# Performance work log

Hardware: AMD Instinct MI355X
Metric: run time of the kernel (lower is better)

## Reference

```python
import jax, jax.numpy as jnp
import numpy as np

B, S, D, H = 2, 2048, 1024, 16
DK = D // H


def setup_inputs() -> dict:
    key = jax.random.key(0)
    ks = jax.random.split(key, 12)
    s = 0.02
    return {
        "q": jax.random.normal(ks[0], (B, S, D), jnp.float32),
        "k": jax.random.normal(ks[1], (B, S, D), jnp.float32),
        "v": jax.random.normal(ks[2], (B, S, D), jnp.float32),
        "mask": jax.random.randint(ks[3], (1, 1, S, S), 0, 2, jnp.int32),
        "Wq": jax.random.normal(ks[4], (D, D), jnp.float32) * s,
        "bq": jnp.zeros((D,), jnp.float32),
        "Wk": jax.random.normal(ks[5], (D, D), jnp.float32) * s,
        "bk": jnp.zeros((D,), jnp.float32),
        "Wv": jax.random.normal(ks[6], (D, D), jnp.float32) * s,
        "bv": jnp.zeros((D,), jnp.float32),
        "Wo": jax.random.normal(ks[7], (D, D), jnp.float32) * s,
        "bo": jnp.zeros((D,), jnp.float32),
    }


def reference(q, k, v, mask, Wq, bq, Wk, bk, Wv, bv, Wo, bo):
    # linear projections (torch Linear: x @ W.T + b)
    qp = q @ Wq.T + bq
    kp = k @ Wk.T + bk
    vp = v @ Wv.T + bv
    # [B, S, D] -> [B, H, S, DK]
    split = lambda x: x.reshape(B, S, H, DK).transpose(0, 2, 1, 3)
    qh, kh, vh = split(qp), split(kp), split(vp)
    scale = 1.0 / jnp.sqrt(jnp.float32(DK))
    attn = jnp.einsum('bhsd,bhtd->bhst', qh, kh) * scale  # [B,H,S,S]
    attn = jnp.where(mask == 0, jnp.float32(-1e9), attn)
    attn = jax.nn.softmax(attn, axis=-1)
    out = jnp.einsum('bhst,bhtd->bhsd', attn, vh)  # [B,H,S,DK]
    concat = out.transpose(0, 2, 1, 3).reshape(B, S, D)
    return concat @ Wo.T + bo
```

## Files before the change

kernel.cpp:

```cpp
#include <hip/hip_runtime.h>
#include <hip/hip_bf16.h>


using bf16x8 = __attribute__((ext_vector_type(8))) short;
using f32x4  = __attribute__((ext_vector_type(4))) float;

constexpr int Bc = 2, Sc = 2048, Dc = 1024, Hc = 16, DKc = 64;
constexpr int Mc = Bc * Sc;
#define QSCALE 0.18033688011112042f

__device__ __forceinline__ void lds_load16(const void* g, void* l) {
  __builtin_amdgcn_global_load_lds(
      (const __attribute__((address_space(1))) unsigned int*)g,
      (__attribute__((address_space(3))) unsigned int*)l, 16, 0, 0);
}

#if __has_builtin(__builtin_amdgcn_exp2f)
__device__ __forceinline__ float exp2_fast(float x) { return __builtin_amdgcn_exp2f(x); }
#else
__device__ __forceinline__ float exp2_fast(float x) {
  float r;
  asm("v_exp_f32 %0, %1\n\ts_nop 0" : "=v"(r) : "v"(x));
  return r;
}
#endif

__device__ __forceinline__ unsigned pack_trunc(float a, float b) {
  return __builtin_amdgcn_perm(__float_as_uint(b), __float_as_uint(a), 0x07060302u);
}

__device__ __forceinline__ unsigned pack2bf(float a, float b) {
  union { __hip_bfloat16 h; unsigned short s; } ua, ub;
  ua.h = __float2bfloat16(a);
  ub.h = __float2bfloat16(b);
  return (unsigned)ua.s | ((unsigned)ub.s << 16);
}

__global__ void prep(const float* __restrict__ q, const float* __restrict__ k,
                     const float* __restrict__ v, const int* __restrict__ mask,
                     const float* __restrict__ Wq, const float* __restrict__ Wk,
                     const float* __restrict__ Wv, const float* __restrict__ Wo,
                     char* __restrict__ ws) {
  const size_t MB = 1024 * 1024;
  int blk = blockIdx.x;
  if (blk < 12288) {
    int which = blk >> 12;
    int i = (((blk & 4095) << 8) + threadIdx.x) * 4;
    const float* s = which == 0 ? q : (which == 1 ? k : v);
    __hip_bfloat16* d = (__hip_bfloat16*)(ws + (size_t)which * 8 * MB);
    float4 x = *(const float4*)&s[i];
    uint2 pk = {pack2bf(x.x, x.y), pack2bf(x.z, x.w)};
    *(uint2*)&d[i] = pk;
  } else if (blk < 16384) {
    int bb = blk - 12288;
    int which = bb >> 10;
    int i = (((bb & 1023) << 8) + threadIdx.x) * 4;
    const float* s = which == 0 ? Wq : (which == 1 ? Wk : (which == 2 ? Wv : Wo));
    __hip_bfloat16* d = which < 3 ? (__hip_bfloat16*)(ws + (24 + 2 * which) * MB)
                                  : (__hip_bfloat16*)(ws + 30 * MB);
    float4 x = *(const float4*)&s[i];
    uint2 pk = {pack2bf(x.x, x.y), pack2bf(x.z, x.w)};
    *(uint2*)&d[i] = pk;
  } else {
    int i = ((blk - 16384) << 8) + threadIdx.x;
    unsigned long long bal = __ballot(mask[i] != 0);
    if ((threadIdx.x & 63) == 0)
      ((unsigned long long*)(ws + 32 * MB))[i >> 6] = bal;
  }
}

__global__ __launch_bounds__(256, 3) void proj_qkv(
    const __hip_bfloat16* __restrict__ qb, const __hip_bfloat16* __restrict__ kb,
    const __hip_bfloat16* __restrict__ vb, const __hip_bfloat16* __restrict__ Wcat,
    const float* __restrict__ bq, const float* __restrict__ bk,
    const float* __restrict__ bv, __hip_bfloat16* __restrict__ qhd,
    __hip_bfloat16* __restrict__ khd, __hip_bfloat16* __restrict__ vtd) {
  __shared__ __align__(16) __hip_bfloat16 As[2][128 * 32];
  __shared__ __align__(16) __hip_bfloat16 Bs[2][128 * 32];
  const int tid = threadIdx.x;
  const int f = blockIdx.x, g = f >> 3;
  const int m0 = ((f & 7) * 4 + g / 24) * 128;
  const int n0 = (g % 24) * 128;
  const int which = n0 >> 10, nl0 = n0 & 1023;
  const __hip_bfloat16* X = which == 0 ? qb : (which == 1 ? kb : vb);
  const float* bias = which == 0 ? bq : (which == 1 ? bk : bv);
  const int w = tid >> 6, lane = tid & 63, ln = lane & 15, quad = lane >> 4;
  const int rl = w * 32 + (lane >> 2);
  const int sw8 = ((lane & 3) ^ ((lane >> 2) & 3)) * 8;
  const int aoff = (n0 + rl) * 1024 + sw8;
  const int boff = (m0 + rl) * 1024 + sw8;
  char* aDst = (char*)As + w * 2048 + lane * 16;
  char* bDst = (char*)Bs + w * 2048 + lane * 16;
  const int rkq = (quad ^ (ln & 3)) * 16;
  const int rA0 = ((w >> 1) * 64 + ln) * 64 + rkq;
  const int rB0 = ((w & 1) * 64 + ln) * 64 + rkq;
  f32x4 acc[4][4] = {};

#define PSTAGE(KO, BI)                                                        \
  {                                                                           \
    lds_load16(&Wcat[aoff + (KO)], aDst + (BI)*8192);                         \
    lds_load16(&Wcat[aoff + 16384 + (KO)], aDst + (BI)*8192 + 1024);          \
    lds_load16(&X[boff + (KO)], bDst + (BI)*8192);                            \
    lds_load16(&X[boff + 16384 + (KO)], bDst + (BI)*8192 + 1024);             \
  }

  PSTAGE(0, 0);
  if (which == 2) {
    for (int kb32 = 0; kb32 < 32; ++kb32) {
      const int bi = kb32 & 1;
      __syncthreads();
      if (kb32 < 31) PSTAGE((kb32 + 1) * 32, bi ^ 1);
      bf16x8 af[4], bf[4];
#pragma unroll
      for (int i = 0; i < 4; ++i)
        af[i] = *(bf16x8*)((char*)As + bi * 8192 + rA0 + i * 1024);
#pragma unroll
      for (int j = 0; j < 4; ++j)
        bf[j] = *(bf16x8*)((char*)Bs + bi * 8192 + rB0 + j * 1024);
#pragma unroll
      for (int i = 0; i < 4; ++i)
#pragma unroll
        for (int j = 0; j < 4; ++j)
          acc[i][j] = __builtin_amdgcn_mfma_f32_16x16x32_bf16(bf[j], af[i],
                                                              acc[i][j], 0, 0, 0);
    }
  } else {
    for (int kb32 = 0; kb32 < 32; ++kb32) {
      const int bi = kb32 & 1;
      __syncthreads();
      if (kb32 < 31) PSTAGE((kb32 + 1) * 32, bi ^ 1);
      bf16x8 af[4], bf[4];
#pragma unroll
      for (int i = 0; i < 4; ++i)
        af[i] = *(bf16x8*)((char*)As + bi * 8192 + rA0 + i * 1024);
#pragma unroll
      for (int j = 0; j < 4; ++j)
        bf[j] = *(bf16x8*)((char*)Bs + bi * 8192 + rB0 + j * 1024);
#pragma unroll
      for (int i = 0; i < 4; ++i)
#pragma unroll
        for (int j = 0; j < 4; ++j)
          acc[i][j] = __builtin_amdgcn_mfma_f32_16x16x32_bf16(af[i], bf[j],
                                                              acc[i][j], 0, 0, 0);
    }
  }

  const int wA = (w >> 1) * 64, wB = (w & 1) * 64;
  if (which == 2) {
#pragma unroll
    for (int i = 0; i < 4; ++i) {
      int nf = nl0 + wA + i * 16 + ln;
      int h = nf >> 6, dk = nf & 63;
      float bb = bias[nf];
#pragma unroll
      for (int j = 0; j < 4; ++j) {
        int sb = m0 + wB + j * 16 + quad * 4;
        int b = sb >> 11, s = sb & 2047;
        float vv[4] = {acc[i][j][0] + bb, acc[i][j][1] + bb,
                       acc[i][j][2] + bb, acc[i][j][3] + bb};
        uint2 pk = {pack2bf(vv[0], vv[1]), pack2bf(vv[2], vv[3])};
        *(uint2*)&vtd[(((size_t)(b * Hc + h) * DKc + dk) * Sc) + s] = pk;
      }
    }
  } else {
#pragma unroll
    for (int i = 0; i < 4; ++i) {
      int nfb = nl0 + wA + i * 16 + quad * 4;
      float4 b4 = *(const float4*)&bias[nfb];
      int h = nfb >> 6, dk0 = nfb & 63;
#pragma unroll
      for (int j = 0; j < 4; ++j) {
        int sg = m0 + wB + j * 16 + ln;
        int b = sg >> 11, s = sg & 2047;
        float vv[4] = {acc[i][j][0] + b4.x, acc[i][j][1] + b4.y,
                       acc[i][j][2] + b4.z, acc[i][j][3] + b4.w};
        if (which == 0) {
          uint2 pk = {pack2bf(vv[0] * QSCALE, vv[1] * QSCALE),
                      pack2bf(vv[2] * QSCALE, vv[3] * QSCALE)};
          *(uint2*)&qhd[(((size_t)(b * Hc + h) * Sc + s) * DKc) + dk0] = pk;
        } else {
          uint2 pk = {pack2bf(vv[0], vv[1]), pack2bf(vv[2], vv[3])};
          *(uint2*)&khd[(((size_t)(b * Hc + h) * Sc + s) * DKc) + dk0] = pk;
        }
      }
    }
  }
}

__global__ __launch_bounds__(256, 2) void gemm_out(
    const __hip_bfloat16* __restrict__ X, const __hip_bfloat16* __restrict__ W,
    const float* __restrict__ bias, float* __restrict__ Y) {
  __shared__ __align__(16) __hip_bfloat16 As[2][64 * 64];
  __shared__ __align__(16) __hip_bfloat16 Bs[2][128 * 64];
  const int tid = threadIdx.x;
  const int f = blockIdx.x, g = f >> 3;
  const int m0 = ((f & 7) * 4 + (g >> 4)) * 128;
  const int n0 = (g & 15) * 64;
  const int w = tid >> 6, lane = tid & 63, ln = lane & 15, quad = lane >> 4;
  const int wA = (w & 1) * 32, wB = (w >> 1) * 64;
  const int swz = ((lane & 7) ^ (lane >> 3)) * 8;
  const int rk0 = ln * 128 + ((quad ^ (ln & 7)) * 16);
  const int rk1 = ln * 128 + (((quad + 4) ^ (ln & 7)) * 16);
  const int aoff = (n0 + w * 16 + (lane >> 3)) * 1024 + swz;
  const int boff = (m0 + w * 32 + (lane >> 3)) * 1024 + swz;
  f32x4 acc[2][4] = {};

#define OSTAGE(KO, BI)                                                        \
  {                                                                           \
    _Pragma("unroll") for (int i = 0; i < 2; ++i)                             \
        lds_load16(&W[aoff + i * 8192 + (KO)],                                \
                   (char*)As[BI] + w * 2048 + lane * 16 + i * 1024);          \
    _Pragma("unroll") for (int i = 0; i < 4; ++i)                             \
        lds_load16(&X[boff + i * 8192 + (KO)],                                \
                   (char*)Bs[BI] + w * 4096 + lane * 16 + i * 1024);          \
  }

  OSTAGE(0, 0);
  for (int kb64 = 0; kb64 < 16; ++kb64) {
    const int bi = kb64 & 1;
    __syncthreads();
    if (kb64 + 1 < 16) OSTAGE((kb64 + 1) * 64, bi ^ 1);
    bf16x8 af[2][2], bf[4][2];
#pragma unroll
    for (int i = 0; i < 2; ++i) {
      af[i][0] = *(bf16x8*)((char*)As[bi] + wA * 128 + i * 2048 + rk0);
      af[i][1] = *(bf16x8*)((char*)As[bi] + wA * 128 + i * 2048 + rk1);
    }
#pragma unroll
    for (int j = 0; j < 4; ++j) {
      bf[j][0] = *(bf16x8*)((char*)Bs[bi] + wB * 128 + j * 2048 + rk0);
      bf[j][1] = *(bf16x8*)((char*)Bs[bi] + wB * 128 + j * 2048 + rk1);
    }
#pragma unroll
    for (int i = 0; i < 2; ++i)
#pragma unroll
      for (int j = 0; j < 4; ++j) {
        acc[i][j] = __builtin_amdgcn_mfma_f32_16x16x32_bf16(af[i][0], bf[j][0],
                                                            acc[i][j], 0, 0, 0);
        acc[i][j] = __builtin_amdgcn_mfma_f32_16x16x32_bf16(af[i][1], bf[j][1],
                                                            acc[i][j], 0, 0, 0);
      }
  }
#pragma unroll
  for (int i = 0; i < 2; ++i) {
    int nfb = n0 + wA + i * 16 + quad * 4;
    float4 b4 = *(const float4*)&bias[nfb];
#pragma unroll
    for (int j = 0; j < 4; ++j) {
      int sg = m0 + wB + j * 16 + ln;
      float4 st = {acc[i][j][0] + b4.x, acc[i][j][1] + b4.y,
                   acc[i][j][2] + b4.z, acc[i][j][3] + b4.w};
      *(float4*)&Y[(size_t)sg * Dc + nfb] = st;
    }
  }
}

__global__ __launch_bounds__(256, 3) void flash_attn(
    const __hip_bfloat16* __restrict__ qh, const __hip_bfloat16* __restrict__ kh,
    const __hip_bfloat16* __restrict__ vt, const uint4* __restrict__ mb4,
    __hip_bfloat16* __restrict__ oc) {
  __shared__ __align__(16) char L[51200];
  const int tid = threadIdx.x;
  const int f = blockIdx.x, g = f >> 3;
  const int bh = (f & 7) * 4 + (g >> 4);
  const int q0 = (g & 15) * 128;
  const int b = bh >> 4, h = bh & 15;
  const int w = tid >> 6, lane = tid & 63, ln = lane & 15, quad = lane >> 4;
  const size_t base = (size_t)bh * Sc * DKc;
  const __hip_bfloat16* khb = kh + base;
  const __hip_bfloat16* vtb = vt + base;

  bf16x8 qf[2][2];
#pragma unroll
  for (int qt = 0; qt < 2; ++qt)
#pragma unroll
    for (int kc = 0; kc < 2; ++kc)
      qf[qt][kc] = *(const bf16x8*)&qh[base +
          (size_t)(q0 + w * 32 + qt * 16 + ln) * 64 + kc * 32 + quad * 8];

  bf16x8 onesA;
#pragma unroll
  for (int i = 0; i < 8; ++i) onesA[i] = (short)0x3F80;

  const int swz = ((lane & 7) ^ (lane >> 3)) * 8;
  const int rk0 = ln * 128 + ((quad ^ (ln & 7)) * 16);
  const int rk1 = ln * 128 + (((quad + 4) ^ (ln & 7)) * 16);
  const int rPw = 32768 + w * 4608 + ln * 144 + quad * 8;
  const int rPb = 32768 + w * 4608 + ln * 144 + quad * 16;
  char* dmaL = L + w * 2048 + lane * 16;
  int koff = (w * 16 + (lane >> 3)) * 64 + swz;
  int voff0 = (w * 16 + (lane >> 3)) * Sc + swz;
  int voff1 = voff0 + 8 * Sc;
  int midx0 = (q0 + w * 32 + ln) * 16;
  int midx1 = midx0 + 256;
  const int sh0 = quad * 4, sh1 = quad * 4 + 16;

#define KV_DMA(BI)                                                            \
  {                                                                           \
    lds_load16(khb + koff, dmaL + (BI)*8192);                                 \
    lds_load16(khb + koff + 512, dmaL + (BI)*8192 + 1024);                    \
    lds_load16(vtb + voff0, dmaL + 16384 + (BI)*8192);                        \
    lds_load16(vtb + voff1, dmaL + 16384 + (BI)*8192 + 1024);                 \
  }

  f32x4 Oacc[4][2] = {};
  f32x4 lacc[2] = {};
  KV_DMA(0);

#define FTILE(BUF, LO0, HI0, LO1, HI1)                                        \
  {                                                                           \
    bf16x8 kf[4][2];                                                          \
    _Pragma("unroll") for (int tt = 0; tt < 4; ++tt) {                        \
      kf[tt][0] = *(bf16x8*)(L + (BUF)*8192 + tt * 2048 + rk0);               \
      kf[tt][1] = *(bf16x8*)(L + (BUF)*8192 + tt * 2048 + rk1);               \
    }                                                                         \
    _Pragma("unroll") for (int qt = 0; qt < 2; ++qt) {                        \
      f32x4 s[4];                                                             \
      _Pragma("unroll") for (int tt = 0; tt < 4; ++tt) {                      \
        f32x4 z = {0.f, 0.f, 0.f, 0.f};                                       \
        z = __builtin_amdgcn_mfma_f32_16x16x32_bf16(kf[tt][0], qf[qt][0], z,  \
                                                    0, 0, 0);                 \
        s[tt] = __builtin_amdgcn_mfma_f32_16x16x32_bf16(kf[tt][1], qf[qt][1], \
                                                        z, 0, 0, 0);          \
      }                                                                       \
      unsigned lo = qt ? (LO1) : (LO0), hi = qt ? (HI1) : (HI0);              \
      _Pragma("unroll") for (int tt = 0; tt < 4; ++tt) {                      \
        unsigned word = (tt & 2) ? hi : lo;                                   \
        unsigned pre = word >> ((tt & 1) ? sh1 : sh0);                        \
        float p[4];                                                           \
        _Pragma("unroll") for (int r = 0; r < 4; ++r) {                       \
          float e = exp2_fast(s[tt][r]);                                      \
          p[r] = (pre & (1u << r)) ? e : 0.f;                                 \
        }                                                                     \
        uint2 pk = {pack_trunc(p[0], p[1]), pack_trunc(p[2], p[3])};          \
        *(uint2*)(L + rPw + qt * 2304 + tt * 32) = pk;                        \
      }                                                                       \
    }                                                                         \
    bf16x8 vf[4][2], pb[2][2];                                                \
    _Pragma("unroll") for (int dt = 0; dt < 4; ++dt) {                        \
      vf[dt][0] = *(bf16x8*)(L + 16384 + (BUF)*8192 + dt * 2048 + rk0);       \
      vf[dt][1] = *(bf16x8*)(L + 16384 + (BUF)*8192 + dt * 2048 + rk1);       \
    }                                                                         \
    _Pragma("unroll") for (int qt = 0; qt < 2; ++qt) {                        \
      pb[qt][0] = *(bf16x8*)(L + rPb + qt * 2304);                            \
      pb[qt][1] = *(bf16x8*)(L + rPb + qt * 2304 + 64);                       \
    }                                                                         \
    _Pragma("unroll") for (int qt = 0; qt < 2; ++qt) {                        \
      lacc[qt] = __builtin_amdgcn_mfma_f32_16x16x32_bf16(onesA, pb[qt][0],    \
                                                         lacc[qt], 0, 0, 0);  \
      lacc[qt] = __builtin_amdgcn_mfma_f32_16x16x32_bf16(onesA, pb[qt][1],    \
                                                         lacc[qt], 0, 0, 0);  \
    }                                                                         \
    _Pragma("unroll") for (int dt = 0; dt < 4; ++dt)                          \
        _Pragma("unroll") for (int qt = 0; qt < 2; ++qt) {                    \
      Oacc[dt][qt] = __builtin_amdgcn_mfma_f32_16x16x32_bf16(                 \
          vf[dt][0], pb[qt][0], Oacc[dt][qt], 0, 0, 0);                       \
      Oacc[dt][qt] = __builtin_amdgcn_mfma_f32_16x16x32_bf16(                 \
          vf[dt][1], pb[qt][1], Oacc[dt][qt], 0, 0, 0);                       \
    }                                                                         \
  }

  for (int it2 = 0; it2 < 16; ++it2) {
    __syncthreads();
    uint4 mq0 = mb4[midx0], mq1 = mb4[midx1];
    ++midx0; ++midx1;
    koff += 4096; voff0 += 64; voff1 += 64;
    KV_DMA(1);
    FTILE(0, mq0.x, mq0.y, mq1.x, mq1.y);
    __syncthreads();
    if (it2 < 15) {
      koff += 4096; voff0 += 64; voff1 += 64;
      KV_DMA(0);
    }
    FTILE(1, mq0.z, mq0.w, mq1.z, mq1.w);
  }

  float linv[2];
#pragma unroll
  for (int qt = 0; qt < 2; ++qt)
    linv[qt] = 1.f / fmaxf(lacc[qt][0], 1e-30f);
#pragma unroll
  for (int dt = 0; dt < 4; ++dt)
#pragma unroll
    for (int qt = 0; qt < 2; ++qt) {
      f32x4 o = Oacc[dt][qt];
      uint2 pk = {pack2bf(o[0] * linv[qt], o[1] * linv[qt]),
                  pack2bf(o[2] * linv[qt], o[3] * linv[qt])};
      *(uint2*)(L + rPw + qt * 2304 + dt * 32) = pk;
    }
  __builtin_amdgcn_s_waitcnt(0);
#pragma unroll
  for (int chunk = 0; chunk < 4; ++chunk) {
    int row = chunk * 8 + (lane >> 3);
    bf16x8 val = *(bf16x8*)(L + 32768 + w * 4608 + row * 144 + (lane & 7) * 16);
    int s = q0 + w * 32 + row;
    *(bf16x8*)&oc[(size_t)(b * Sc + s) * Dc + h * 64 + (lane & 7) * 8] = val;
  }
}

extern "C" void kernel_launch(void* const* d_in, const int* in_sizes, int n_in,
                              void* d_out, int out_size, void* d_ws, size_t ws_size,
                              hipStream_t stream) {
  const float* q  = (const float*)d_in[0];
  const float* k  = (const float*)d_in[1];
  const float* v  = (const float*)d_in[2];
  const int* mask = (const int*)d_in[3];
  const float* Wq = (const float*)d_in[4];
  const float* bq = (const float*)d_in[5];
  const float* Wk = (const float*)d_in[6];
  const float* bk = (const float*)d_in[7];
  const float* Wv = (const float*)d_in[8];
  const float* bv = (const float*)d_in[9];
  const float* Wo = (const float*)d_in[10];
  const float* bo = (const float*)d_in[11];

  char* ws = (char*)d_ws;
  const size_t MB = 1024 * 1024;
  __hip_bfloat16* qb   = (__hip_bfloat16*)(ws + 0 * MB);
  __hip_bfloat16* kb   = (__hip_bfloat16*)(ws + 8 * MB);
  __hip_bfloat16* vb   = (__hip_bfloat16*)(ws + 16 * MB);
  __hip_bfloat16* Wcat = (__hip_bfloat16*)(ws + 24 * MB);
  __hip_bfloat16* Wob  = (__hip_bfloat16*)(ws + 30 * MB);
  uint4*          mb4  = (uint4*)(ws + 32 * MB);
  __hip_bfloat16* qhd  = (__hip_bfloat16*)(ws + 33 * MB);
  __hip_bfloat16* khd  = (__hip_bfloat16*)(ws + 41 * MB);
  __hip_bfloat16* vtd  = (__hip_bfloat16*)(ws + 49 * MB);
  __hip_bfloat16* oc   = (__hip_bfloat16*)(ws + 57 * MB);

  prep<<<32768, 256, 0, stream>>>(q, k, v, mask, Wq, Wk, Wv, Wo, ws);
  proj_qkv<<<768, 256, 0, stream>>>(qb, kb, vb, Wcat, bq, bk, bv, qhd, khd, vtd);
  flash_attn<<<512, 256, 0, stream>>>(qhd, khd, vtd, mb4, oc);
  gemm_out<<<512, 256, 0, stream>>>(oc, Wob, bo, (float*)d_out);
}
```

Measured before the change: 246.2 us.

## Split KV range across two wave groups per attention block with LDS reduction

The flash attention block doubles to 512 threads, made of two groups of four waves. Each group processes alternating 64-key tiles of the same query rows, which doubles the waves resident per CU. Group 1 then spills its partial O accumulator and row sums to LDS, and group 0 adds them in before normalising and writing the output. The K and V loads are also re-phased: one buffer per group instead of a double buffer, with the V load issued at loop start and the next K load issued after the score phase. This may expose more load latency, and LDS use grows to about 68 KB per block.

New measurement: 250.9 us. About the same (+1.9%).

```diff
diff --git a/kernel.cpp b/kernel.cpp
--- a/kernel.cpp
+++ b/kernel.cpp
@@ -255,17 +255,18 @@
   }
 }
 
-__global__ __launch_bounds__(256, 3) void flash_attn(
+__global__ __launch_bounds__(512, 4) void flash_attn(
     const __hip_bfloat16* __restrict__ qh, const __hip_bfloat16* __restrict__ kh,
     const __hip_bfloat16* __restrict__ vt, const uint4* __restrict__ mb4,
     __hip_bfloat16* __restrict__ oc) {
-  __shared__ __align__(16) char L[51200];
+  __shared__ __align__(16) char L[69632];
   const int tid = threadIdx.x;
   const int f = blockIdx.x, g = f >> 3;
   const int bh = (f & 7) * 4 + (g >> 4);
   const int q0 = (g & 15) * 128;
   const int b = bh >> 4, h = bh & 15;
   const int w = tid >> 6, lane = tid & 63, ln = lane & 15, quad = lane >> 4;
+  const int grp = w >> 2, wl = w & 3;
   const size_t base = (size_t)bh * Sc * DKc;
   const __hip_bfloat16* khb = kh + base;
   const __hip_bfloat16* vtb = vt + base;
@@ -276,7 +277,7 @@
 #pragma unroll
     for (int kc = 0; kc < 2; ++kc)
       qf[qt][kc] = *(const bf16x8*)&qh[base +
-          (size_t)(q0 + w * 32 + qt * 16 + ln) * 64 + kc * 32 + quad * 8];
+          (size_t)(q0 + wl * 32 + qt * 16 + ln) * 64 + kc * 32 + quad * 8];
 
   bf16x8 onesA;
 #pragma unroll
@@ -287,115 +288,154 @@
   const int rk1 = ln * 128 + (((quad + 4) ^ (ln & 7)) * 16);
   const int rPw = 32768 + w * 4608 + ln * 144 + quad * 8;
   const int rPb = 32768 + w * 4608 + ln * 144 + quad * 16;
-  char* dmaL = L + w * 2048 + lane * 16;
-  int koff = (w * 16 + (lane >> 3)) * 64 + swz;
-  int voff0 = (w * 16 + (lane >> 3)) * Sc + swz;
+  const int KB = grp * 8192, VB = 16384 + grp * 8192;
+  char* kdma = L + KB + wl * 2048 + lane * 16;
+  char* vdma = L + VB + wl * 2048 + lane * 16;
+  int koff = (grp * 64 + wl * 16 + (lane >> 3)) * 64 + swz;
+  int voff0 = (wl * 16 + (lane >> 3)) * Sc + swz + grp * 64;
   int voff1 = voff0 + 8 * Sc;
-  int midx0 = (q0 + w * 32 + ln) * 16;
+  int midx0 = (q0 + wl * 32 + ln) * 16;
   int midx1 = midx0 + 256;
   const int sh0 = quad * 4, sh1 = quad * 4 + 16;
 
-#define KV_DMA(BI)                                                            \
+#define K_DMA()                                                               \
   {                                                                           \
-    lds_load16(khb + koff, dmaL + (BI)*8192);                                 \
-    lds_load16(khb + koff + 512, dmaL + (BI)*8192 + 1024);                    \
-    lds_load16(vtb + voff0, dmaL + 16384 + (BI)*8192);                        \
-    lds_load16(vtb + voff1, dmaL + 16384 + (BI)*8192 + 1024);                 \
+    lds_load16(khb + koff, kdma);                                             \
+    lds_load16(khb + koff + 512, kdma + 1024);                                \
+  }
+#define V_DMA()                                                               \
+  {                                                                           \
+    lds_load16(vtb + voff0, vdma);                                            \
+    lds_load16(vtb + voff1, vdma + 1024);                                     \
   }
 
   f32x4 Oacc[4][2] = {};
   f32x4 lacc[2] = {};
-  KV_DMA(0);
-
-#define FTILE(BUF, LO0, HI0, LO1, HI1)                                        \
-  {                                                                           \
-    bf16x8 kf[4][2];                                                          \
-    _Pragma("unroll") for (int tt = 0; tt < 4; ++tt) {                        \
-      kf[tt][0] = *(bf16x8*)(L + (BUF)*8192 + tt * 2048 + rk0);               \
-      kf[tt][1] = *(bf16x8*)(L + (BUF)*8192 + tt * 2048 + rk1);               \
-    }                                                                         \
-    _Pragma("unroll") for (int qt = 0; qt < 2; ++qt) {                        \
-      f32x4 s[4];                                                             \
-      _Pragma("unroll") for (int tt = 0; tt < 4; ++tt) {                      \
-        f32x4 z = {0.f, 0.f, 0.f, 0.f};                                       \
-        z = __builtin_amdgcn_mfma_f32_16x16x32_bf16(kf[tt][0], qf[qt][0], z,  \
-                                                    0, 0, 0);                 \
-        s[tt] = __builtin_amdgcn_mfma_f32_16x16x32_bf16(kf[tt][1], qf[qt][1], \
-                                                        z, 0, 0, 0);          \
-      }                                                                       \
-      unsigned lo = qt ? (LO1) : (LO0), hi = qt ? (HI1) : (HI0);              \
-      _Pragma("unroll") for (int tt = 0; tt < 4; ++tt) {                      \
-        unsigned word = (tt & 2) ? hi : lo;                                   \
-        unsigned pre = word >> ((tt & 1) ? sh1 : sh0);                        \
-        float p[4];                                                           \
-        _Pragma("unroll") for (int r = 0; r < 4; ++r) {                       \
-          float e = exp2_fast(s[tt][r]);                                      \
-          p[r] = (pre & (1u << r)) ? e : 0.f;                                 \
-        }                                                                     \
-        uint2 pk = {pack_trunc(p[0], p[1]), pack_trunc(p[2], p[3])};          \
-        *(uint2*)(L + rPw + qt * 2304 + tt * 32) = pk;                        \
-      }                                                                       \
-    }                                                                         \
-    bf16x8 vf[4][2], pb[2][2];                                                \
-    _Pragma("unroll") for (int dt = 0; dt < 4; ++dt) {                        \
-      vf[dt][0] = *(bf16x8*)(L + 16384 + (BUF)*8192 + dt * 2048 + rk0);       \
-      vf[dt][1] = *(bf16x8*)(L + 16384 + (BUF)*8192 + dt * 2048 + rk1);       \
-    }                                                                         \
-    _Pragma("unroll") for (int qt = 0; qt < 2; ++qt) {                        \
-      pb[qt][0] = *(bf16x8*)(L + rPb + qt * 2304);                            \
-      pb[qt][1] = *(bf16x8*)(L + rPb + qt * 2304 + 64);                       \
-    }                                                                         \
-    _Pragma("unroll") for (int qt = 0; qt < 2; ++qt) {                        \
-      lacc[qt] = __builtin_amdgcn_mfma_f32_16x16x32_bf16(onesA, pb[qt][0],    \
-                                                         lacc[qt], 0, 0, 0);  \
-      lacc[qt] = __builtin_amdgcn_mfma_f32_16x16x32_bf16(onesA, pb[qt][1],    \
-                                                         lacc[qt], 0, 0, 0);  \
-    }                                                                         \
-    _Pragma("unroll") for (int dt = 0; dt < 4; ++dt)                          \
-        _Pragma("unroll") for (int qt = 0; qt < 2; ++qt) {                    \
-      Oacc[dt][qt] = __builtin_amdgcn_mfma_f32_16x16x32_bf16(                 \
-          vf[dt][0], pb[qt][0], Oacc[dt][qt], 0, 0, 0);                       \
-      Oacc[dt][qt] = __builtin_amdgcn_mfma_f32_16x16x32_bf16(                 \
-          vf[dt][1], pb[qt][1], Oacc[dt][qt], 0, 0, 0);                       \
-    }                                                                         \
-  }
-
-  for (int it2 = 0; it2 < 16; ++it2) {
+  K_DMA();
+  V_DMA();
+
+  for (int r = 0; r < 16; ++r) {
     __syncthreads();
+    if (r > 0) { voff0 += 128; voff1 += 128; V_DMA(); }
     uint4 mq0 = mb4[midx0], mq1 = mb4[midx1];
     ++midx0; ++midx1;
-    koff += 4096; voff0 += 64; voff1 += 64;
-    KV_DMA(1);
-    FTILE(0, mq0.x, mq0.y, mq1.x, mq1.y);
+    const unsigned lo0 = grp ? mq0.z : mq0.x, hi0 = grp ? mq0.w : mq0.y;
+    const unsigned lo1 = grp ? mq1.z : mq1.x, hi1 = grp ? mq1.w : mq1.y;
+
+    bf16x8 kf[4][2];
+#pragma unroll
+    for (int tt = 0; tt < 4; ++tt) {
+      kf[tt][0] = *(bf16x8*)(L + KB + tt * 2048 + rk0);
+      kf[tt][1] = *(bf16x8*)(L + KB + tt * 2048 + rk1);
+    }
+#pragma unroll
+    for (int qt = 0; qt < 2; ++qt) {
+      f32x4 s4[4];
+#pragma unroll
+      for (int tt = 0; tt < 4; ++tt) {
+        f32x4 z = {0.f, 0.f, 0.f, 0.f};
+        z = __builtin_amdgcn_mfma_f32_16x16x32_bf16(kf[tt][0], qf[qt][0], z,
+                                                    0, 0, 0);
+        s4[tt] = __builtin_amdgcn_mfma_f32_16x16x32_bf16(kf[tt][1], qf[qt][1],
+                                                         z, 0, 0, 0);
+      }
+      const unsigned lo = qt ? lo1 : lo0, hi = qt ? hi1 : hi0;
+#pragma unroll
+      for (int tt = 0; tt < 4; ++tt) {
+        unsigned word = (tt & 2) ? hi : lo;
+        unsigned pre = word >> ((tt & 1) ? sh1 : sh0);
+        float p[4];
+#pragma unroll
+        for (int rr = 0; rr < 4; ++rr) {
+          float e = exp2_fast(s4[tt][rr]);
+          p[rr] = (pre & (1u << rr)) ? e : 0.f;
+        }
+        uint2 pk = {pack_trunc(p[0], p[1]), pack_trunc(p[2], p[3])};
+        *(uint2*)(L + rPw + qt * 2304 + tt * 32) = pk;
+      }
+    }
+
     __syncthreads();
-    if (it2 < 15) {
-      koff += 4096; voff0 += 64; voff1 += 64;
-      KV_DMA(0);
-    }
-    FTILE(1, mq0.z, mq0.w, mq1.z, mq1.w);
-  }
-
-  float linv[2];
-#pragma unroll
-  for (int qt = 0; qt < 2; ++qt)
-    linv[qt] = 1.f / fmaxf(lacc[qt][0], 1e-30f);
-#pragma unroll
-  for (int dt = 0; dt < 4; ++dt)
+    if (r < 15) { koff += 8192; K_DMA(); }
+
+    bf16x8 vf[4][2], pb[2][2];
+#pragma unroll
+    for (int dt = 0; dt < 4; ++dt) {
+      vf[dt][0] = *(bf16x8*)(L + VB + dt * 2048 + rk0);
+      vf[dt][1] = *(bf16x8*)(L + VB + dt * 2048 + rk1);
+    }
 #pragma unroll
     for (int qt = 0; qt < 2; ++qt) {
-      f32x4 o = Oacc[dt][qt];
-      uint2 pk = {pack2bf(o[0] * linv[qt], o[1] * linv[qt]),
-                  pack2bf(o[2] * linv[qt], o[3] * linv[qt])};
-      *(uint2*)(L + rPw + qt * 2304 + dt * 32) = pk;
-    }
-  __builtin_amdgcn_s_waitcnt(0);
-#pragma unroll
-  for (int chunk = 0; chunk < 4; ++chunk) {
-    int row = chunk * 8 + (lane >> 3);
-    bf16x8 val = *(bf16x8*)(L + 32768 + w * 4608 + row * 144 + (lane & 7) * 16);
-    int s = q0 + w * 32 + row;
-    *(bf16x8*)&oc[(size_t)(b * Sc + s) * Dc + h * 64 + (lane & 7) * 8] = val;
-  }
+      pb[qt][0] = *(bf16x8*)(L + rPb + qt * 2304);
+      pb[qt][1] = *(bf16x8*)(L + rPb + qt * 2304 + 64);
+    }
+#pragma unroll
+    for (int qt = 0; qt < 2; ++qt) {
+      lacc[qt] = __builtin_amdgcn_mfma_f32_16x16x32_bf16(onesA, pb[qt][0],
+                                                         lacc[qt], 0, 0, 0);
+      lacc[qt] = __builtin_amdgcn_mfma_f32_16x16x32_bf16(onesA, pb[qt][1],
+                                                         lacc[qt], 0, 0, 0);
+    }
+#pragma unroll
+    for (int dt = 0; dt < 4; ++dt)
+#pragma unroll
+      for (int qt = 0; qt < 2; ++qt) {
+        Oacc[dt][qt] = __builtin_amdgcn_mfma_f32_16x16x32_bf16(
+            vf[dt][0], pb[qt][0], Oacc[dt][qt], 0, 0, 0);
+        Oacc[dt][qt] = __builtin_amdgcn_mfma_f32_16x16x32_bf16(
+            vf[dt][1], pb[qt][1], Oacc[dt][qt], 0, 0, 0);
+      }
+  }
+
+  __syncthreads();
+  if (grp == 1) {
+#pragma unroll
+    for (int dt = 0; dt < 4; ++dt)
+#pragma unroll
+      for (int qt = 0; qt < 2; ++qt) {
+        int slot = (dt * 4 + quad) ^ ln;
+        *(f32x4*)(L + wl * 8192 + (qt * 16 + ln) * 256 + slot * 16) =
+            Oacc[dt][qt];
+      }
+    if (quad == 0) {
+      *(float*)(L + 65536 + wl * 128 + ln * 4) = lacc[0][0];
+      *(float*)(L + 65536 + wl * 128 + 64 + ln * 4) = lacc[1][0];
+    }
+  }
+  __syncthreads();
+  if (grp == 0) {
+    float linv[2];
+#pragma unroll
+    for (int qt = 0; qt < 2; ++qt) {
+      float lsum = lacc[qt][0] +
+                   *(float*)(L + 65536 + wl * 128 + qt * 64 + ln * 4);
+      linv[qt] = 1.f / fmaxf(lsum, 1e-30f);
+    }
+#pragma unroll
+    for (int dt = 0; dt < 4; ++dt)
+#pragma unroll
+      for (int qt = 0; qt < 2; ++qt) {
+        int slot = (dt * 4 + quad) ^ ln;
+        f32x4 part =
+            *(f32x4*)(L + wl * 8192 + (qt * 16 + ln) * 256 + slot * 16);
+        f32x4 o = Oacc[dt][qt];
+        o[0] += part[0]; o[1] += part[1]; o[2] += part[2]; o[3] += part[3];
+        uint2 pk = {pack2bf(o[0] * linv[qt], o[1] * linv[qt]),
+                    pack2bf(o[2] * linv[qt], o[3] * linv[qt])};
+        *(uint2*)(L + rPw + qt * 2304 + dt * 32) = pk;
+      }
+    __builtin_amdgcn_s_waitcnt(0);
+#pragma unroll
+    for (int chunk = 0; chunk < 4; ++chunk) {
+      int row = chunk * 8 + (lane >> 3);
+      bf16x8 val =
+          *(bf16x8*)(L + 32768 + w * 4608 + row * 144 + (lane & 7) * 16);
+      int s = q0 + w * 32 + row;
+      *(bf16x8*)&oc[(size_t)(b * Sc + s) * Dc + h * 64 + (lane & 7) * 8] = val;
+    }
+  }
+#undef K_DMA
+#undef V_DMA
 }
 
 extern "C" void kernel_launch(void* const* d_in, const int* in_sizes, int n_in,
@@ -429,6 +469,6 @@
 
   prep<<<32768, 256, 0, stream>>>(q, k, v, mask, Wq, Wk, Wv, Wo, ws);
   proj_qkv<<<768, 256, 0, stream>>>(qb, kb, vb, Wcat, bq, bk, bv, qhd, khd, vtd);
-  flash_attn<<<512, 256, 0, stream>>>(qhd, khd, vtd, mb4, oc);
+  flash_attn<<<512, 512, 0, stream>>>(qhd, khd, vtd, mb4, oc);
   gemm_out<<<512, 256, 0, stream>>>(oc, Wob, bo, (float*)d_out);
 }
```
